# Kernel tuning notes

Hardware: AMD Instinct MI355X
Metric: run time of the kernel (lower is better)

## Reference

```python
import jax, jax.numpy as jnp
import numpy as np

EPS = 1e-8

def _conv(x, w, b=None):
    # NCHW conv, stride 1, SAME padding (k=3, pad=1)
    y = jax.lax.conv_general_dilated(x, w, (1, 1), 'SAME',
                                     dimension_numbers=('NCHW', 'OIHW', 'NCHW'))
    if b is not None:
        y = y + b[None, :, None, None]
    return y

def setup_inputs() -> dict:
    key = jax.random.key(0)
    ks = jax.random.split(key, 6)
    B, C, H, W = 512, 1024, 8, 8
    return {
        'x': jax.random.normal(ks[0], (B, C, H, W), jnp.float32),
        'w1_1': jax.random.normal(ks[1], (1, 1, 3, 3), jnp.float32) * 0.1,
        'w5': jax.random.normal(ks[2], (4, 2, 3, 3), jnp.float32) * 0.1,
        'b5': jax.random.normal(ks[3], (4,), jnp.float32) * 0.1,
        'w6': jax.random.normal(ks[4], (1, 4, 3, 3), jnp.float32) * 0.1,
        'b6': jax.random.normal(ks[5], (1,), jnp.float32) * 0.1,
    }

def reference(x, w1_1, w5, b5, w6, b6):
    B, C, H, W = x.shape  # H == W == 8 by module construction
    m = jnp.max(x, axis=1, keepdims=True)  # [B,1,H,W] channel max
    # 2x2 non-overlapping windows, torch unfold layout -> [B,1,(H/2)*(W/2),4]
    win = m.reshape(B, 1, H // 2, 2, W // 2, 2)
    win = win.transpose(0, 1, 2, 4, 3, 5).reshape(B, 1, (H // 2) * (W // 2), 4)
    # probabilistic pooling: clean inf/nan/negatives, sample per window
    winc = jnp.where(jnp.isinf(win) | jnp.isnan(win) | (win < 0), EPS, win)
    skey = jax.random.key(1)
    idx = jax.random.categorical(skey, winc, axis=-1)  # softmax(winc) multinomial
    mo2 = jnp.take_along_axis(winc, idx[..., None], axis=-1)[..., 0]
    mo2 = mo2.reshape(B, 1, H // 2, W // 2)
    # adaptive max/avg pool (4,4) on 8x8 == 2x2 pooling, reuse windows
    mo3 = win.max(axis=-1).reshape(B, 1, H // 2, W // 2)
    ao4 = win.mean(axis=-1).reshape(B, 1, H // 2, W // 2)
    out2 = 0.1 * mo2 + 0.6 * mo3 + 0.3 * ao4
    out2 = _conv(out2, w1_1)  # bias-free 1->1 conv
    out2 = jax.image.resize(out2, (B, 1, H, W), method='bilinear')  # align_corners=False
    out1 = jnp.concatenate([m, out2], axis=1)  # [B,2,H,W]
    gate = jax.nn.sigmoid(_conv(jax.nn.relu(_conv(out1, w5, b5)), w6, b6))  # [B,1,H,W]
    return jax.nn.relu(x * gate)
```

## Files before the change

kernel.cpp:

```cpp
#include <hip/hip_runtime.h>
#include <math.h>

#define C_DIM 1024
#define HW 64
#define NT 1024
#define F4B 16384
#define PER_T 16
#define EPSV 1e-8f
#define TINYF 1.17549435e-38f

typedef float f32x4_t __attribute__((ext_vector_type(4)));

__device__ __forceinline__ void keepf(float v) { asm volatile("" :: "v"(v)); }

__device__ __forceinline__ void threefry2x32_01(unsigned x0, unsigned x1,
                                                unsigned& o0, unsigned& o1) {
    const unsigned ks0 = 0u, ks1 = 1u, ks2 = 0x1BD11BDBu;
    x0 += ks0; x1 += ks1;
#define TF_R(r) { x0 += x1; x1 = (x1 << (r)) | (x1 >> (32 - (r))); x1 ^= x0; }
    TF_R(13) TF_R(15) TF_R(26) TF_R(6)
    x0 += ks1; x1 += ks2 + 1u;
    TF_R(17) TF_R(29) TF_R(16) TF_R(24)
    x0 += ks2; x1 += ks0 + 2u;
    TF_R(13) TF_R(15) TF_R(26) TF_R(6)
    x0 += ks0; x1 += ks1 + 3u;
    TF_R(17) TF_R(29) TF_R(16) TF_R(24)
    x0 += ks1; x1 += ks2 + 4u;
    TF_R(13) TF_R(15) TF_R(26) TF_R(6)
    x0 += ks2; x1 += ks0 + 5u;
#undef TF_R
    o0 = x0; o1 = x1;
}

__device__ __forceinline__ unsigned jax_random_bits(unsigned n) {
    unsigned o0, o1;
    threefry2x32_01(0u, n, o0, o1);
    return o0 ^ o1;
}

__device__ __forceinline__ float gumbel01(unsigned n) {
    unsigned bits = jax_random_bits(n);
    float f = __uint_as_float(0x3F800000u | (bits >> 9)) - 1.0f;
    float u = fmaxf(TINYF, f + TINYF);
    return -logf(-logf(u));
}

__device__ __forceinline__ bool bad_val(float v) {
    return ((__float_as_uint(v) & 0x7F800000u) == 0x7F800000u) || (v < 0.0f);
}

__device__ __forceinline__ void middle_net(
    int t, float sgum,
    const float4* __restrict__ red,
    const float* __restrict__ w11, const float* __restrict__ w5,
    const float* __restrict__ b5, const float* __restrict__ w6,
    const float* __restrict__ b6,
    float* sm, float* sa16, float* sb16, float* so2, float* shid,
    float* sgate)
{
    {
        int g = t & 15, set = t >> 4;
        float4 a = red[(set * 4 + 0) * 16 + g];
#pragma unroll
        for (int w = 1; w < 4; ++w) {
            float4 o = red[(set * 4 + w) * 16 + g];
            a.x = fmaxf(a.x, o.x); a.y = fmaxf(a.y, o.y);
            a.z = fmaxf(a.z, o.z); a.w = fmaxf(a.w, o.w);
        }
#pragma unroll
        for (int off = 16; off <= 32; off <<= 1) {
            a.x = fmaxf(a.x, __shfl_xor(a.x, off, 64));
            a.y = fmaxf(a.y, __shfl_xor(a.y, off, 64));
            a.z = fmaxf(a.z, __shfl_xor(a.z, off, 64));
            a.w = fmaxf(a.w, __shfl_xor(a.w, off, 64));
        }
        if (t < 16) {
            sm[t * 4 + 0] = a.x; sm[t * 4 + 1] = a.y;
            sm[t * 4 + 2] = a.z; sm[t * 4 + 3] = a.w;
        }
    }
    __builtin_amdgcn_wave_barrier();

    {
        int w = t >> 2, j = t & 3;
        int hh = 2 * (w >> 2) + (j >> 1), ww = 2 * (w & 3) + (j & 1);
        float v = sm[hh * 8 + ww];
        float wc = bad_val(v) ? EPSV : v;
        float s = wc + sgum;
        int bi = j;
        float bwc = wc;
        float mx = v;
        float ssum = v;
#pragma unroll
        for (int m = 1; m <= 2; m <<= 1) {
            float s2   = __shfl_xor(s, m, 64);
            int   bi2  = __shfl_xor(bi, m, 64);
            float bwc2 = __shfl_xor(bwc, m, 64);
            float mx2  = __shfl_xor(mx, m, 64);
            float ss2  = __shfl_xor(ssum, m, 64);
            bool take = (s2 > s) || (s2 == s && bi2 < bi);
            if (take) { s = s2; bi = bi2; bwc = bwc2; }
            mx = fmaxf(mx, mx2);
            ssum += ss2;
        }
        if (j == 0) sa16[w] = 0.1f * bwc + 0.6f * mx + 0.3f * (ssum * 0.25f);
    }
    __builtin_amdgcn_wave_barrier();

    if (t < 16) {
        int i = t >> 2, j = t & 3;
        float acc = 0.0f;
#pragma unroll
        for (int dy = -1; dy <= 1; ++dy) {
            int yy = i + dy;
            if (yy < 0 || yy > 3) continue;
#pragma unroll
            for (int dx = -1; dx <= 1; ++dx) {
                int xx = j + dx;
                if (xx < 0 || xx > 3) continue;
                acc += sa16[yy * 4 + xx] * w11[(dy + 1) * 3 + (dx + 1)];
            }
        }
        sb16[t] = acc;
    }
    __builtin_amdgcn_wave_barrier();

    {
        int y = t >> 3, xx2 = t & 7;
        float sy = (y + 0.5f) * 0.5f - 0.5f;
        float sx = (xx2 + 0.5f) * 0.5f - 0.5f;
        float fy = fminf(fmaxf(sy, 0.0f), 3.0f);
        float fx = fminf(fmaxf(sx, 0.0f), 3.0f);
        int iy0 = (int)floorf(fy); int iy1 = min(iy0 + 1, 3); float ry = fy - (float)iy0;
        int ix0 = (int)floorf(fx); int ix1 = min(ix0 + 1, 3); float rx = fx - (float)ix0;
        float v00 = sb16[iy0 * 4 + ix0], v01 = sb16[iy0 * 4 + ix1];
        float v10 = sb16[iy1 * 4 + ix0], v11 = sb16[iy1 * 4 + ix1];
        float top = v00 * (1.0f - rx) + v01 * rx;
        float bot = v10 * (1.0f - rx) + v11 * rx;
        so2[t] = top * (1.0f - ry) + bot * ry;
    }
    __builtin_amdgcn_wave_barrier();

    {
        int y = t >> 3, x2 = t & 7;
        float a0 = b5[0], a1 = b5[1], a2 = b5[2], a3 = b5[3];
#pragma unroll
        for (int dy = -1; dy <= 1; ++dy) {
            int yy = y + dy;
            if (yy < 0 || yy > 7) continue;
#pragma unroll
            for (int dx = -1; dx <= 1; ++dx) {
                int xx = x2 + dx;
                if (xx < 0 || xx > 7) continue;
                float i0 = sm[yy * 8 + xx];
                float i1 = so2[yy * 8 + xx];
                int kk = (dy + 1) * 3 + (dx + 1);
                a0 += i0 * w5[0 * 18 + kk] + i1 * w5[0 * 18 + 9 + kk];
                a1 += i0 * w5[1 * 18 + kk] + i1 * w5[1 * 18 + 9 + kk];
                a2 += i0 * w5[2 * 18 + kk] + i1 * w5[2 * 18 + 9 + kk];
                a3 += i0 * w5[3 * 18 + kk] + i1 * w5[3 * 18 + 9 + kk];
            }
        }
        shid[0 * 64 + t] = fmaxf(a0, 0.0f);
        shid[1 * 64 + t] = fmaxf(a1, 0.0f);
        shid[2 * 64 + t] = fmaxf(a2, 0.0f);
        shid[3 * 64 + t] = fmaxf(a3, 0.0f);
    }
    __builtin_amdgcn_wave_barrier();

    {
        int y = t >> 3, x2 = t & 7;
        float acc = b6[0];
#pragma unroll
        for (int dy = -1; dy <= 1; ++dy) {
            int yy = y + dy;
            if (yy < 0 || yy > 7) continue;
#pragma unroll
            for (int dx = -1; dx <= 1; ++dx) {
                int xx = x2 + dx;
                if (xx < 0 || xx > 7) continue;
                int kk = (dy + 1) * 3 + (dx + 1);
                int p = yy * 8 + xx;
                acc += shid[0 * 64 + p] * w6[0 + kk]
                     + shid[1 * 64 + p] * w6[9 + kk]
                     + shid[2 * 64 + p] * w6[18 + kk]
                     + shid[3 * 64 + p] * w6[27 + kk];
            }
        }
        sgate[t] = 1.0f / (1.0f + expf(-acc));
    }
}

__global__ __launch_bounds__(NT) void sa_fused_kernel(
    const float* __restrict__ x,
    const float* __restrict__ w11,
    const float* __restrict__ w5,
    const float* __restrict__ b5,
    const float* __restrict__ w6,
    const float* __restrict__ b6,
    float* __restrict__ out)
{
    const int bid = blockIdx.x;
    const int t = threadIdx.x;
    const int half = gridDim.x;
    const int b0 = bid, b1 = bid + half;
    const int wv = t >> 6, lane = t & 63;

    const float4* __restrict__ x4 = (const float4*)x;
    const float4* __restrict__ xb0 = x4 + (size_t)b0 * F4B;
    const float4* __restrict__ xb1 = x4 + (size_t)b1 * F4B;
    float4* __restrict__ ob0 = (float4*)out + (size_t)b0 * F4B;
    float4* __restrict__ ob1 = (float4*)out + (size_t)b1 * F4B;

    __shared__ float4 red0[16 * 16];
    __shared__ float4 red1[16 * 16];
    __shared__ float sm[64], sa16[16], sb16[16], so2[64], shid[4 * 64];
    __shared__ __align__(16) float sgate0[64];
    __shared__ __align__(16) float sgate1[64];

    float4 xv[PER_T];
#pragma unroll
    for (int i = 0; i < PER_T; ++i) xv[i] = xb0[t + NT * i];
    if (t == 0) {
        keepf(w11[0]); keepf(w5[0]); keepf(w5[32]); keepf(w5[64]);
        keepf(b5[0]);  keepf(w6[0]); keepf(w6[32]); keepf(b6[0]);
    }
    const float sgum0 = gumbel01((unsigned)(b0 * 64 + lane));
    float4 pm = make_float4(-INFINITY, -INFINITY, -INFINITY, -INFINITY);
#pragma unroll
    for (int i = 0; i < PER_T; ++i) {
        pm.x = fmaxf(pm.x, xv[i].x); pm.y = fmaxf(pm.y, xv[i].y);
        pm.z = fmaxf(pm.z, xv[i].z); pm.w = fmaxf(pm.w, xv[i].w);
    }
#pragma unroll
    for (int off = 16; off <= 32; off <<= 1) {
        pm.x = fmaxf(pm.x, __shfl_xor(pm.x, off, 64));
        pm.y = fmaxf(pm.y, __shfl_xor(pm.y, off, 64));
        pm.z = fmaxf(pm.z, __shfl_xor(pm.z, off, 64));
        pm.w = fmaxf(pm.w, __shfl_xor(pm.w, off, 64));
    }
    if (lane < 16) red0[wv * 16 + lane] = pm;
    __syncthreads();

    float4 yv[PER_T];
#pragma unroll
    for (int i = 0; i < PER_T; ++i) yv[i] = xb1[t + NT * i];
    const float sgum1 = gumbel01((unsigned)(b1 * 64 + lane));
    if (t < 64)
        middle_net(t, sgum0, red0, w11, w5, b5, w6, b6,
                   sm, sa16, sb16, so2, shid, sgate0);
    pm = make_float4(-INFINITY, -INFINITY, -INFINITY, -INFINITY);
#pragma unroll
    for (int i = 0; i < PER_T; ++i) {
        pm.x = fmaxf(pm.x, yv[i].x); pm.y = fmaxf(pm.y, yv[i].y);
        pm.z = fmaxf(pm.z, yv[i].z); pm.w = fmaxf(pm.w, yv[i].w);
    }
#pragma unroll
    for (int off = 16; off <= 32; off <<= 1) {
        pm.x = fmaxf(pm.x, __shfl_xor(pm.x, off, 64));
        pm.y = fmaxf(pm.y, __shfl_xor(pm.y, off, 64));
        pm.z = fmaxf(pm.z, __shfl_xor(pm.z, off, 64));
        pm.w = fmaxf(pm.w, __shfl_xor(pm.w, off, 64));
    }
    if (lane < 16) red1[wv * 16 + lane] = pm;
    __syncthreads();

    if (t < 64)
        middle_net(t, sgum1, red1, w11, w5, b5, w6, b6,
                   sm, sa16, sb16, so2, shid, sgate1);
    {
        const float4 g0 = ((const float4*)sgate0)[t & 15];
#pragma unroll
        for (int i = 0; i < PER_T; ++i) {
            float4 v = xb0[t + NT * i];
            f32x4_t o;
            o.x = fmaxf(v.x * g0.x, 0.0f);
            o.y = fmaxf(v.y * g0.y, 0.0f);
            o.z = fmaxf(v.z * g0.z, 0.0f);
            o.w = fmaxf(v.w * g0.w, 0.0f);
            __builtin_nontemporal_store(o, (f32x4_t*)&ob0[t + NT * i]);
        }
    }
    __syncthreads();

    {
        const float4 g1 = ((const float4*)sgate1)[t & 15];
#pragma unroll
        for (int i = 0; i < PER_T; ++i) {
            float4 v = xb1[t + NT * i];
            f32x4_t o;
            o.x = fmaxf(v.x * g1.x, 0.0f);
            o.y = fmaxf(v.y * g1.y, 0.0f);
            o.z = fmaxf(v.z * g1.z, 0.0f);
            o.w = fmaxf(v.w * g1.w, 0.0f);
            __builtin_nontemporal_store(o, (f32x4_t*)&ob1[t + NT * i]);
        }
    }
}

extern "C" void kernel_launch(void* const* d_in, const int* in_sizes, int n_in,
                              void* d_out, int out_size, void* d_ws, size_t ws_size,
                              hipStream_t stream) {
    const float* x   = (const float*)d_in[0];
    const float* w11 = (const float*)d_in[1];
    const float* w5  = (const float*)d_in[2];
    const float* b5  = (const float*)d_in[3];
    const float* w6  = (const float*)d_in[4];
    const float* b6  = (const float*)d_in[5];
    float* out  = (float*)d_out;

    int B = in_sizes[0] / (C_DIM * HW);
    sa_fused_kernel<<<dim3(B / 2), dim3(NT), 0, stream>>>(x, w11, w5, b5, w6, b6, out);
}
```

Measured before the change: 263.9 us.

## Restructure two-batch pipeline to interleave second-batch max with first-batch output

```diff
diff --git a/kernel.cpp b/kernel.cpp
--- a/kernel.cpp
+++ b/kernel.cpp
@@ -10,8 +10,6 @@
 #define TINYF 1.17549435e-38f
 
 typedef float f32x4_t __attribute__((ext_vector_type(4)));
-
-__device__ __forceinline__ void keepf(float v) { asm volatile("" :: "v"(v)); }
 
 __device__ __forceinline__ void threefry2x32_01(unsigned x0, unsigned x1,
                                                 unsigned& o0, unsigned& o1) {
@@ -38,19 +36,12 @@
     return o0 ^ o1;
 }
 
-__device__ __forceinline__ float gumbel01(unsigned n) {
-    unsigned bits = jax_random_bits(n);
-    float f = __uint_as_float(0x3F800000u | (bits >> 9)) - 1.0f;
-    float u = fmaxf(TINYF, f + TINYF);
-    return -logf(-logf(u));
-}
-
 __device__ __forceinline__ bool bad_val(float v) {
     return ((__float_as_uint(v) & 0x7F800000u) == 0x7F800000u) || (v < 0.0f);
 }
 
 __device__ __forceinline__ void middle_net(
-    int t, float sgum,
+    int t, int b,
     const float4* __restrict__ red,
     const float* __restrict__ w11, const float* __restrict__ w5,
     const float* __restrict__ b5, const float* __restrict__ w6,
@@ -86,7 +77,11 @@
         int hh = 2 * (w >> 2) + (j >> 1), ww = 2 * (w & 3) + (j & 1);
         float v = sm[hh * 8 + ww];
         float wc = bad_val(v) ? EPSV : v;
-        float s = wc + sgum;
+        unsigned bits = jax_random_bits((unsigned)(b * 64 + t));
+        float f = __uint_as_float(0x3F800000u | (bits >> 9)) - 1.0f;
+        float u = fmaxf(TINYF, f + TINYF);
+        float sg = -logf(-logf(u));
+        float s = wc + sg;
         int bi = j;
         float bwc = wc;
         float mx = v;
@@ -191,7 +186,7 @@
     }
 }
 
-__global__ __launch_bounds__(NT) void sa_fused_kernel(
+__global__ __launch_bounds__(NT) void sa_fused2_kernel(
     const float* __restrict__ x,
     const float* __restrict__ w11,
     const float* __restrict__ w5,
@@ -202,35 +197,25 @@
 {
     const int bid = blockIdx.x;
     const int t = threadIdx.x;
-    const int half = gridDim.x;
-    const int b0 = bid, b1 = bid + half;
+    const int b0 = bid * 2, b1 = b0 + 1;
     const int wv = t >> 6, lane = t & 63;
 
-    const float4* __restrict__ x4 = (const float4*)x;
-    const float4* __restrict__ xb0 = x4 + (size_t)b0 * F4B;
-    const float4* __restrict__ xb1 = x4 + (size_t)b1 * F4B;
+    const float4* __restrict__ xb0 = (const float4*)x + (size_t)b0 * F4B;
+    const float4* __restrict__ xb1 = (const float4*)x + (size_t)b1 * F4B;
     float4* __restrict__ ob0 = (float4*)out + (size_t)b0 * F4B;
     float4* __restrict__ ob1 = (float4*)out + (size_t)b1 * F4B;
 
-    __shared__ float4 red0[16 * 16];
-    __shared__ float4 red1[16 * 16];
+    __shared__ float4 red[16 * 16];
     __shared__ float sm[64], sa16[16], sb16[16], so2[64], shid[4 * 64];
     __shared__ __align__(16) float sgate0[64];
     __shared__ __align__(16) float sgate1[64];
 
-    float4 xv[PER_T];
-#pragma unroll
-    for (int i = 0; i < PER_T; ++i) xv[i] = xb0[t + NT * i];
-    if (t == 0) {
-        keepf(w11[0]); keepf(w5[0]); keepf(w5[32]); keepf(w5[64]);
-        keepf(b5[0]);  keepf(w6[0]); keepf(w6[32]); keepf(b6[0]);
-    }
-    const float sgum0 = gumbel01((unsigned)(b0 * 64 + lane));
     float4 pm = make_float4(-INFINITY, -INFINITY, -INFINITY, -INFINITY);
 #pragma unroll
     for (int i = 0; i < PER_T; ++i) {
-        pm.x = fmaxf(pm.x, xv[i].x); pm.y = fmaxf(pm.y, xv[i].y);
-        pm.z = fmaxf(pm.z, xv[i].z); pm.w = fmaxf(pm.w, xv[i].w);
+        float4 v = xb0[t + NT * i];
+        pm.x = fmaxf(pm.x, v.x); pm.y = fmaxf(pm.y, v.y);
+        pm.z = fmaxf(pm.z, v.z); pm.w = fmaxf(pm.w, v.w);
     }
 #pragma unroll
     for (int off = 16; off <= 32; off <<= 1) {
@@ -239,53 +224,49 @@
         pm.z = fmaxf(pm.z, __shfl_xor(pm.z, off, 64));
         pm.w = fmaxf(pm.w, __shfl_xor(pm.w, off, 64));
     }
-    if (lane < 16) red0[wv * 16 + lane] = pm;
-    __syncthreads();
-
-    float4 yv[PER_T];
-#pragma unroll
-    for (int i = 0; i < PER_T; ++i) yv[i] = xb1[t + NT * i];
-    const float sgum1 = gumbel01((unsigned)(b1 * 64 + lane));
+    if (lane < 16) red[wv * 16 + lane] = pm;
+    __syncthreads();
+
     if (t < 64)
-        middle_net(t, sgum0, red0, w11, w5, b5, w6, b6,
+        middle_net(t, b0, red, w11, w5, b5, w6, b6,
                    sm, sa16, sb16, so2, shid, sgate0);
-    pm = make_float4(-INFINITY, -INFINITY, -INFINITY, -INFINITY);
-#pragma unroll
-    for (int i = 0; i < PER_T; ++i) {
-        pm.x = fmaxf(pm.x, yv[i].x); pm.y = fmaxf(pm.y, yv[i].y);
-        pm.z = fmaxf(pm.z, yv[i].z); pm.w = fmaxf(pm.w, yv[i].w);
-    }
-#pragma unroll
-    for (int off = 16; off <= 32; off <<= 1) {
-        pm.x = fmaxf(pm.x, __shfl_xor(pm.x, off, 64));
-        pm.y = fmaxf(pm.y, __shfl_xor(pm.y, off, 64));
-        pm.z = fmaxf(pm.z, __shfl_xor(pm.z, off, 64));
-        pm.w = fmaxf(pm.w, __shfl_xor(pm.w, off, 64));
-    }
-    if (lane < 16) red1[wv * 16 + lane] = pm;
+    __syncthreads();
+
+    {
+        const float4 g0 = ((const float4*)sgate0)[t & 15];
+        pm = make_float4(-INFINITY, -INFINITY, -INFINITY, -INFINITY);
+#pragma unroll 4
+        for (int i = 0; i < PER_T; ++i) {
+            float4 v1 = xb1[t + NT * i];
+            float4 v0 = xb0[t + NT * i];
+            pm.x = fmaxf(pm.x, v1.x); pm.y = fmaxf(pm.y, v1.y);
+            pm.z = fmaxf(pm.z, v1.z); pm.w = fmaxf(pm.w, v1.w);
+            f32x4_t o;
+            o.x = fmaxf(v0.x * g0.x, 0.0f);
+            o.y = fmaxf(v0.y * g0.y, 0.0f);
+            o.z = fmaxf(v0.z * g0.z, 0.0f);
+            o.w = fmaxf(v0.w * g0.w, 0.0f);
+            __builtin_nontemporal_store(o, (f32x4_t*)&ob0[t + NT * i]);
+        }
+#pragma unroll
+        for (int off = 16; off <= 32; off <<= 1) {
+            pm.x = fmaxf(pm.x, __shfl_xor(pm.x, off, 64));
+            pm.y = fmaxf(pm.y, __shfl_xor(pm.y, off, 64));
+            pm.z = fmaxf(pm.z, __shfl_xor(pm.z, off, 64));
+            pm.w = fmaxf(pm.w, __shfl_xor(pm.w, off, 64));
+        }
+        if (lane < 16) red[wv * 16 + lane] = pm;
+    }
     __syncthreads();
 
     if (t < 64)
-        middle_net(t, sgum1, red1, w11, w5, b5, w6, b6,
+        middle_net(t, b1, red, w11, w5, b5, w6, b6,
                    sm, sa16, sb16, so2, shid, sgate1);
-    {
-        const float4 g0 = ((const float4*)sgate0)[t & 15];
-#pragma unroll
-        for (int i = 0; i < PER_T; ++i) {
-            float4 v = xb0[t + NT * i];
-            f32x4_t o;
-            o.x = fmaxf(v.x * g0.x, 0.0f);
-            o.y = fmaxf(v.y * g0.y, 0.0f);
-            o.z = fmaxf(v.z * g0.z, 0.0f);
-            o.w = fmaxf(v.w * g0.w, 0.0f);
-            __builtin_nontemporal_store(o, (f32x4_t*)&ob0[t + NT * i]);
-        }
-    }
     __syncthreads();
 
     {
         const float4 g1 = ((const float4*)sgate1)[t & 15];
-#pragma unroll
+#pragma unroll 4
         for (int i = 0; i < PER_T; ++i) {
             float4 v = xb1[t + NT * i];
             f32x4_t o;
@@ -310,5 +291,6 @@
     float* out  = (float*)d_out;
 
     int B = in_sizes[0] / (C_DIM * HW);
-    sa_fused_kernel<<<dim3(B / 2), dim3(NT), 0, stream>>>(x, w11, w5, b5, w6, b6, out);
-}
+    sa_fused2_kernel<<<dim3(B / 2), dim3(NT), 0, stream>>>(
+        x, w11, w5, b5, w6, b6, out);
+}
```

After: 256.2 us. 1.03x faster.
